# Kernel optimization log

Hardware: AMD Instinct MI355X
Metric: run time of the kernel (lower is better)

The kernel has to match this reference:

```python
import jax, jax.numpy as jnp
import numpy as np
import math

D = 256
N = 2048
B = 8
N_PLUS_1 = 2048  # masked index (1-based) in the score matrix


def setup_inputs() -> dict:
    key = jax.random.key(0)
    k1, k2, k3, k4, k5 = jax.random.split(key, 5)
    scale = 1.0 / math.sqrt(D)
    return {
        "Z_in": jax.random.normal(k1, (B, D + 1, N), dtype=jnp.float32),
        "A_l": jax.random.normal(k2, (D, D), dtype=jnp.float32) * scale,
        "r_l": jax.random.normal(k3, (1,), dtype=jnp.float32),
        "B_l": jax.random.normal(k4, (D, D), dtype=jnp.float32) * scale,
        "C_l": jax.random.normal(k5, (D, D), dtype=jnp.float32) * scale,
    }


def reference(Z_in, A_l, r_l, B_l, C_l):
    # Z_in: (B, d+1, N)
    X = Z_in[:, :D, :]   # (B, d, N)
    Y = Z_in[:, D:, :]   # (B, 1, N)
    U = jnp.einsum('ij,bjn->bin', B_l, X)  # (B, d, N)
    W = jnp.einsum('ij,bjn->bin', C_l, X)  # (B, d, N)
    scores = jnp.einsum('bdn,bdm->bnm', U, W)  # (B, N, N) = U^T W
    att = jax.nn.relu(scores)                  # h_type == 'relu'
    # zero the (n_plus_1-1, n_plus_1-1) diagonal entry of the attention core
    att = att.at[:, N_PLUS_1 - 1, N_PLUS_1 - 1].set(0.0)
    X_att = jnp.einsum('bdn,bnm->bdm', X, att)  # (B, d, N)
    X_out = X + jnp.einsum('ij,bjm->bim', A_l, X_att)
    Y_out = Y + r_l * jnp.einsum('bdn,bnm->bdm', Y, att)
    return jnp.concatenate([X_out, Y_out], axis=1)  # (B, d+1, N)
```

## Files before the change

### kernel.cpp

```cpp
#include <hip/hip_runtime.h>

#define D 256
#define N 2048
#define NB 8
#define ZSTRIDE (257 * 2048)

typedef __attribute__((ext_vector_type(8))) short short8;
typedef __attribute__((ext_vector_type(4))) short short4v;
typedef __attribute__((ext_vector_type(4))) float f32x4;

#define MFMA(a, b, c) __builtin_amdgcn_mfma_f32_16x16x32_bf16((a), (b), (c), 0, 0, 0)

#define GLOAD_LDS16(g, s) __builtin_amdgcn_global_load_lds( \
    (const __attribute__((address_space(1))) void*)(g),     \
    (__attribute__((address_space(3))) void*)(s), 16, 0, 0)

#define VMCNT(Nstr) asm volatile("s_waitcnt vmcnt(" Nstr ")" ::: "memory")
#define BAR() __builtin_amdgcn_s_barrier()

__device__ __forceinline__ short f2bf(float f) {
    unsigned u = __builtin_bit_cast(unsigned, f);
    u += 0x7fffu + ((u >> 16) & 1u);
    return (short)(u >> 16);
}
__device__ __forceinline__ float bf2f(short s) {
    unsigned u = ((unsigned)(unsigned short)s) << 16;
    return __builtin_bit_cast(float, u);
}

__global__ __launch_bounds__(256) void prep_small(
    const float* __restrict__ B_l, const float* __restrict__ C_l,
    const float* __restrict__ A_l, const float* __restrict__ Z,
    short* __restrict__ G, short* __restrict__ Ab, short* __restrict__ Yb,
    float* __restrict__ accY, int zeroAcc)
{
    int blk = blockIdx.x, tid = threadIdx.x;
    if (blk < 256) {
        float s = 0.f;
        #pragma unroll 8
        for (int k = 0; k < 256; ++k)
            s += B_l[k * 256 + blk] * C_l[k * 256 + tid];
        G[blk * 256 + tid] = f2bf(s);
    } else if (blk < 320) {
        int base = (blk - 256) * 1024 + tid;
        #pragma unroll
        for (int r = 0; r < 4; ++r) {
            int idx = base + r * 256;
            Ab[idx] = f2bf(A_l[idx]);
        }
    } else if (blk < 336) {
        int base = (blk - 320) * 1024 + tid;
        #pragma unroll
        for (int r = 0; r < 4; ++r) {
            int idx = base + r * 256;
            int b = idx >> 11, n = idx & 2047;
            Yb[idx] = f2bf(Z[(size_t)b * ZSTRIDE + 256 * N + n]);
        }
    } else if (zeroAcc) {
        int i = (blk - 336) * 256 + tid;
        f32x4 z = {0.f, 0.f, 0.f, 0.f};
        *(f32x4*)(accY + (size_t)i * 4) = z;
    }
}

__global__ __launch_bounds__(256) void transpose_kernel(
    const float* __restrict__ Z, short* __restrict__ Xt)
{
    typedef __attribute__((ext_vector_type(4))) float f4;
    __shared__ short t[64][68];
    int blk = blockIdx.x;
    int b = blk & 7;
    int dt = (blk >> 3) & 3;
    int nt = blk >> 5;
    int d0 = dt * 64, n0 = nt * 64;
    const float* ZB = Z + (size_t)b * ZSTRIDE;
    int tid = threadIdx.x;
    #pragma unroll
    for (int k = 0; k < 4; ++k) {
        int f = tid + k * 256;
        int r = f >> 4, c4 = f & 15;
        f4 v = *(const f4*)(ZB + (size_t)(d0 + r) * N + n0 + c4 * 4);
        #pragma unroll
        for (int j = 0; j < 4; ++j) t[r][c4 * 4 + j] = f2bf(v[j]);
    }
    __syncthreads();
    short* XtB = Xt + (size_t)b * (N * D);
    #pragma unroll
    for (int k = 0; k < 2; ++k) {
        int f = tid + k * 256;
        int n = f >> 3, c8 = f & 7;
        short8 v;
        #pragma unroll
        for (int j = 0; j < 8; ++j) v[j] = t[c8 * 8 + j][n];
        *(short8*)(XtB + (size_t)(n0 + n) * D + d0 + c8 * 8) = v;
    }
}

__global__ __launch_bounds__(512, 4) void prep_gemm2(
    const short* __restrict__ Xt, const short* __restrict__ G,
    const short* __restrict__ Ab, short* __restrict__ Wt, short* __restrict__ Px)
{
    __shared__ __align__(16) char smem[65536];
    typedef short TileT[128][64];
    TileT* As = (TileT*)smem;
    TileT* Bs = (TileT*)(smem + 32768);

    int blk = blockIdx.x;
    int half = blk >> 8;
    int r0 = blk & 255;
    int b = r0 >> 5;
    int idx = r0 & 31;

    const short* Arows;
    const short* Brows;
    short* Cout;
    size_t cstride;
    int row_base, col_base;
    if (half == 0) {
        row_base = (idx & 15) << 7;
        col_base = (idx >> 4) << 7;
        Arows = Xt + (size_t)b * (N * D);
        Brows = G;
        Cout  = Wt + (size_t)b * (N * D);
        cstride = D;
    } else {
        row_base = (idx & 1) << 7;
        col_base = (idx >> 1) << 7;
        Arows = Ab;
        Brows = Xt + (size_t)b * (N * D);
        Cout  = Px + (size_t)b * (D * N);
        cstride = N;
    }

    int tid = threadIdx.x;
    int w = tid >> 6, l = tid & 63;
    int l16 = l & 15, lq = l >> 4;
    int wm = w >> 2, wn = w & 3;
    int lrow8 = l >> 3, lc = l & 7;

    auto STAGE = [&](const short* base, int row0g, int kt, TileT* dst) {
        #pragma unroll
        for (int i = 0; i < 2; ++i) {
            int rloc = i * 64 + w * 8;
            int row = rloc + lrow8;
            const char* src = (const char*)(base + (size_t)(row0g + row) * D)
                              + kt * 128 + ((lc ^ (row & 7)) * 16);
            GLOAD_LDS16(src, &(*dst)[rloc][0]);
        }
    };

    f32x4 zero4 = {0.f, 0.f, 0.f, 0.f};
    f32x4 acc[4][2];
    #pragma unroll
    for (int mi = 0; mi < 4; ++mi)
        #pragma unroll
        for (int ni = 0; ni < 2; ++ni) acc[mi][ni] = zero4;

    STAGE(Arows, row_base, 0, &As[0]);
    STAGE(Brows, col_base, 0, &Bs[0]);

    int buf = 0;
    #pragma unroll
    for (int kt = 0; kt < 4; ++kt) {
        if (kt < 3) {
            STAGE(Arows, row_base, kt + 1, &As[buf ^ 1]);
            STAGE(Brows, col_base, kt + 1, &Bs[buf ^ 1]);
            VMCNT("4");
        } else {
            VMCNT("0");
        }
        BAR();
        __builtin_amdgcn_s_setprio(1);
        #pragma unroll
        for (int ks = 0; ks < 2; ++ks) {
            short8 af[4], bf[2];
            #pragma unroll
            for (int mi = 0; mi < 4; ++mi) {
                int r = wm * 64 + mi * 16 + l16;
                af[mi] = *(const short8*)(&As[buf][r][(ks * 32 + lq * 8) ^ ((r & 7) << 3)]);
            }
            #pragma unroll
            for (int ni = 0; ni < 2; ++ni) {
                int r = wn * 32 + ni * 16 + l16;
                bf[ni] = *(const short8*)(&Bs[buf][r][(ks * 32 + lq * 8) ^ ((r & 7) << 3)]);
            }
            #pragma unroll
            for (int mi = 0; mi < 4; ++mi)
                #pragma unroll
                for (int ni = 0; ni < 2; ++ni)
                    acc[mi][ni] = MFMA(af[mi], bf[ni], acc[mi][ni]);
        }
        __builtin_amdgcn_s_setprio(0);
        BAR();
        buf ^= 1;
    }

    short* cq = (short*)smem + (size_t)w * (64 * 40);
    #pragma unroll
    for (int mi = 0; mi < 4; ++mi)
        #pragma unroll
        for (int ni = 0; ni < 2; ++ni)
            #pragma unroll
            for (int rg = 0; rg < 4; ++rg)
                cq[(mi * 16 + lq * 4 + rg) * 40 + ni * 16 + l16] =
                    f2bf(acc[mi][ni][rg]);
    #pragma unroll
    for (int p = 0; p < 4; ++p) {
        int row = p * 16 + (l >> 2), c8 = l & 3;
        short8 v = *(const short8*)(&cq[row * 40 + c8 * 8]);
        *(short8*)(Cout + (size_t)(row_base + wm * 64 + row) * cstride +
                   col_base + wn * 32 + c8 * 8) = v;
    }
}

__global__ __launch_bounds__(512, 4) void scores_kernel(
    const short* __restrict__ Xt, const short* __restrict__ Wt,
    const short* __restrict__ Yb, short* __restrict__ attT,
    float* __restrict__ accY, int bBase, int nbMask, int nbShift)
{
    __shared__ __align__(16) char smem[77824];
    typedef short ATile[128][32];
    typedef short BTile[256][32];
    ATile* As = (ATile*)smem;
    BTile* Bs = (BTile*)(smem + 16384);
    short* scratch = (short*)(smem + 49152);

    int blk = blockIdx.x;
    int b_local = blk & nbMask;
    int idx = blk >> nbShift;
    int m_base = (idx & 15) << 7;
    int nsup = (idx >> 4) << 9;
    int b = bBase + b_local;

    int tid = threadIdx.x;
    int w = tid >> 6, l = tid & 63;
    int l16 = l & 15, lq = l >> 4;
    int wm = w >> 2, wn = w & 3;
    int lr4 = l >> 2, lc4 = l & 3;

    const short* WtB = Wt + (size_t)b * (N * D);
    const short* XtB = Xt + (size_t)b * (N * D);
    const short* YbB = Yb + (size_t)b * N;
    float* accYB = accY + (size_t)b * N;
    short* attTB = attT + (size_t)b_local * N * N;

    auto STAGE_A = [&](int kt, int bi) {
        int row = w * 16 + lr4;
        const char* src = (const char*)(WtB + (size_t)(m_base + row) * D)
                          + kt * 64 + ((lc4 ^ ((row >> 1) & 3)) * 16);
        GLOAD_LDS16(src, &As[bi][w * 16][0]);
    };
    auto STAGE_B = [&](int s, int kt, int bi) {
        #pragma unroll
        for (int i = 0; i < 2; ++i) {
            int row = i * 128 + w * 16 + lr4;
            const char* src = (const char*)(XtB + (size_t)(nsup + s * 256 + row) * D)
                              + kt * 64 + ((lc4 ^ ((row >> 1) & 3)) * 16);
            GLOAD_LDS16(src, &Bs[bi][i * 128 + w * 16][0]);
        }
    };

    f32x4 zero4 = {0.f, 0.f, 0.f, 0.f};
    f32x4 acc[4][4];
    #pragma unroll
    for (int mi = 0; mi < 4; ++mi)
        #pragma unroll
        for (int ni = 0; ni < 4; ++ni) acc[mi][ni] = zero4;

    STAGE_A(0, 0);
    STAGE_B(0, 0, 0);

    for (int t = 0; t < 16; ++t) {
        int kt = t & 7;
        int s = t >> 3;
        int buf = t & 1;
        if (t < 15) {
            int t1 = t + 1;
            STAGE_A(t1 & 7, t1 & 1);
            STAGE_B(t1 >> 3, t1 & 7, t1 & 1);
            VMCNT("3");
        } else {
            VMCNT("0");
        }
        BAR();
        __builtin_amdgcn_s_setprio(1);
        {
            short8 af[4], bf[4];
            #pragma unroll
            for (int mi = 0; mi < 4; ++mi) {
                int r = wm * 64 + mi * 16 + l16;
                af[mi] = *(const short8*)(&As[buf][r][(lq ^ ((r >> 1) & 3)) * 8]);
            }
            #pragma unroll
            for (int ni = 0; ni < 4; ++ni) {
                int r = wn * 64 + ni * 16 + l16;
                bf[ni] = *(const short8*)(&Bs[buf][r][(lq ^ ((r >> 1) & 3)) * 8]);
            }
            #pragma unroll
            for (int mi = 0; mi < 4; ++mi)
                #pragma unroll
                for (int ni = 0; ni < 4; ++ni)
                    acc[mi][ni] = MFMA(af[mi], bf[ni], acc[mi][ni]);
        }
        __builtin_amdgcn_s_setprio(0);
        BAR();

        if (kt == 7) {
            int n_base = nsup + s * 256;
            bool corner = (m_base == 1920) && (n_base == 1792);
            #pragma unroll
            for (int mi = 0; mi < 4; ++mi)
                #pragma unroll
                for (int ni = 0; ni < 4; ++ni)
                    #pragma unroll
                    for (int rg = 0; rg < 4; ++rg) {
                        float v = acc[mi][ni][rg];
                        v = v > 0.f ? v : 0.f;
                        if (corner) {
                            int gm = m_base + wm * 64 + mi * 16 + lq * 4 + rg;
                            int gn = n_base + wn * 64 + ni * 16 + l16;
                            if (gm == N - 1 && gn == N - 1) v = 0.f;
                        }
                        acc[mi][ni][rg] = v;
                    }
            {
                float yv[4];
                #pragma unroll
                for (int ni = 0; ni < 4; ++ni)
                    yv[ni] = bf2f(YbB[n_base + wn * 64 + ni * 16 + l16]);
                #pragma unroll
                for (int mi = 0; mi < 4; ++mi)
                    #pragma unroll
                    for (int rg = 0; rg < 4; ++rg) {
                        float sY = acc[mi][0][rg] * yv[0] + acc[mi][1][rg] * yv[1]
                                 + acc[mi][2][rg] * yv[2] + acc[mi][3][rg] * yv[3];
                        sY += __shfl_xor(sY, 1);
                        sY += __shfl_xor(sY, 2);
                        sY += __shfl_xor(sY, 4);
                        sY += __shfl_xor(sY, 8);
                        if (l16 == 0)
                            atomicAdd(&accYB[m_base + wm * 64 + mi * 16 + lq * 4 + rg], sY);
                    }
            }
            {
                short* sq = scratch + (size_t)w * (64 * 28);
                #pragma unroll
                for (int h = 0; h < 4; ++h) {
                    #pragma unroll
                    for (int mi = 0; mi < 4; ++mi)
                        #pragma unroll
                        for (int rg = 0; rg < 4; ++rg)
                            sq[(mi * 16 + lq * 4 + rg) * 28 + l16] =
                                f2bf(acc[mi][h][rg]);
                    #pragma unroll
                    for (int p = 0; p < 2; ++p) {
                        int row = p * 32 + (l >> 1), c8 = l & 1;
                        short8 v = *(const short8*)(&sq[row * 28 + c8 * 8]);
                        *(short8*)(attTB + (size_t)(m_base + wm * 64 + row) * N +
                                   n_base + wn * 64 + h * 16 + c8 * 8) = v;
                    }
                }
            }
            #pragma unroll
            for (int mi = 0; mi < 4; ++mi)
                #pragma unroll
                for (int ni = 0; ni < 4; ++ni) acc[mi][ni] = zero4;
        }
    }
}

__global__ __launch_bounds__(512, 4) void pv_kernel(
    const float* __restrict__ Z, const short* __restrict__ Px,
    const short* __restrict__ attT, const float* __restrict__ accY,
    const float* __restrict__ r_l, float* __restrict__ out,
    int bBase, int nbMask, int nbShift)
{
    __shared__ __align__(16) char smem[49152];
    typedef short ATile[64][64];
    typedef short BTile[128][64];
    ATile* As = (ATile*)smem;
    BTile* Bs = (BTile*)(smem + 16384);

    int blk = blockIdx.x;
    int b_local = blk & nbMask;
    int idx = blk >> nbShift;
    int d_base = (idx & 3) << 6;
    int m_base = (idx >> 2) << 7;
    int b = bBase + b_local;

    int tid = threadIdx.x;
    int w = tid >> 6, l = tid & 63;
    int l16 = l & 15, lq = l >> 4;
    int wd = w >> 2, wm = w & 3;
    int lrow8 = l >> 3, lc = l & 7;

    const short* PxB = Px + (size_t)b * (D * N);
    const short* attTB = attT + (size_t)b_local * N * N;

    auto STAGE_A = [&](int kt, ATile* dst) {
        int rloc = w * 8;
        int row = rloc + lrow8;
        const char* src = (const char*)(PxB + (size_t)(d_base + row) * N)
                          + kt * 128 + ((lc ^ (row & 7)) * 16);
        GLOAD_LDS16(src, &(*dst)[rloc][0]);
    };
    auto STAGE_B = [&](int kt, BTile* dst) {
        #pragma unroll
        for (int i = 0; i < 2; ++i) {
            int rloc = i * 64 + w * 8;
            int row = rloc + lrow8;
            const char* src = (const char*)(attTB + (size_t)(m_base + row) * N)
                              + kt * 128 + ((lc ^ (row & 7)) * 16);
            GLOAD_LDS16(src, &(*dst)[rloc][0]);
        }
    };

    f32x4 zero4 = {0.f, 0.f, 0.f, 0.f};
    f32x4 acc[2][2];
    #pragma unroll
    for (int di = 0; di < 2; ++di)
        #pragma unroll
        for (int mj = 0; mj < 2; ++mj) acc[di][mj] = zero4;

    STAGE_A(0, &As[0]);
    STAGE_B(0, &Bs[0]);

    int buf = 0;
    for (int kt = 0; kt < 32; ++kt) {
        if (kt < 31) {
            STAGE_A(kt + 1, &As[buf ^ 1]);
            STAGE_B(kt + 1, &Bs[buf ^ 1]);
            VMCNT("3");
        } else {
            VMCNT("0");
        }
        BAR();
        __builtin_amdgcn_s_setprio(1);
        #pragma unroll
        for (int ks = 0; ks < 2; ++ks) {
            short8 af[2], bf[2];
            #pragma unroll
            for (int di = 0; di < 2; ++di) {
                int r = wd * 32 + di * 16 + l16;
                af[di] = *(const short8*)(&As[buf][r][(ks * 32 + lq * 8) ^ ((r & 7) << 3)]);
            }
            #pragma unroll
            for (int mj = 0; mj < 2; ++mj) {
                int r = wm * 32 + mj * 16 + l16;
                bf[mj] = *(const short8*)(&Bs[buf][r][(ks * 32 + lq * 8) ^ ((r & 7) << 3)]);
            }
            #pragma unroll
            for (int di = 0; di < 2; ++di)
                #pragma unroll
                for (int mj = 0; mj < 2; ++mj)
                    acc[di][mj] = MFMA(af[di], bf[mj], acc[di][mj]);
        }
        __builtin_amdgcn_s_setprio(0);
        BAR();
        buf ^= 1;
    }

    #pragma unroll
    for (int di = 0; di < 2; ++di)
        #pragma unroll
        for (int mj = 0; mj < 2; ++mj)
            #pragma unroll
            for (int rg = 0; rg < 4; ++rg) {
                int dd = d_base + wd * 32 + di * 16 + lq * 4 + rg;
                int mm = m_base + wm * 32 + mj * 16 + l16;
                size_t off = (size_t)b * ZSTRIDE + (size_t)dd * N + mm;
                out[off] = Z[off] + acc[di][mj][rg];
            }

    if (d_base == 0 && tid < 128) {
        int mm = m_base + tid;
        size_t off = (size_t)b * ZSTRIDE + (size_t)256 * N + mm;
        out[off] = Z[off] + r_l[0] * accY[(size_t)b * N + mm];
    }
}

__global__ __launch_bounds__(512, 4) void fused_kernel(
    const float* __restrict__ Z, const short* __restrict__ Xt,
    const short* __restrict__ Wt, const short* __restrict__ Px,
    const short* __restrict__ Yb, const float* __restrict__ r_l,
    float* __restrict__ out)
{
    __shared__ __align__(16) short xtsA[32][256];
    __shared__ __align__(16) short xtsB[32][256];
    __shared__ __align__(16) short attA[64][36];
    __shared__ __align__(16) short attB[64][36];

    int blk = blockIdx.x;
    int b = blk & 7;
    int m_base = (blk >> 3) << 6;
    int tid = threadIdx.x;
    int w = tid >> 6, l = tid & 63;
    int l16 = l & 15, lq = l >> 4;

    const short* XtB = Xt + (size_t)b * (N * D);
    const short* WtB = Wt + (size_t)b * (N * D);
    const short* PxB = Px + (size_t)b * (D * N);
    const short* YbB = Yb + b * N;

    int mi = w >> 1;
    int nj = w & 1;

    short8 a_wt[8];
    {
        const short* ap = WtB + (size_t)(m_base + 16 * mi + l16) * D + lq * 8;
        #pragma unroll
        for (int ks = 0; ks < 8; ++ks)
            a_wt[ks] = *(const short8*)(ap + ks * 32);
    }

    f32x4 zero4 = {0.f, 0.f, 0.f, 0.f};
    f32x4 accX[2][4];
    #pragma unroll
    for (int di = 0; di < 2; ++di)
        #pragma unroll
        for (int mj = 0; mj < 4; ++mj) accX[di][mj] = zero4;

    float accY = 0.f;
    int ym = tid >> 3, yseg = tid & 7;

    auto STAGE = [&](int it, short (*dst)[256]) {
        #pragma unroll
        for (int r = 0; r < 2; ++r) {
            int row  = r * 16 + 2 * w + (l >> 5);
            int colb = ((l & 31) * 16) ^ ((row & 7) << 4);
            const char* src = (const char*)(XtB + (size_t)(it * 32 + row) * D) + colb;
            GLOAD_LDS16(src, &dst[r * 16 + 2 * w][0]);
        }
    };

    auto BODY = [&](int it, short (*xrd)[256], short (*xst)[256], short (*atw)[36]) {
        int n_base = it * 32;
        if (it + 1 < 64) STAGE(it + 1, xst);
        short8 px[2];
        #pragma unroll
        for (int di = 0; di < 2; ++di)
            px[di] = *(const short8*)(PxB + (size_t)(32 * w + 16 * di + l16) * N +
                                      n_base + lq * 8);
        short4v yv = *(const short4v*)(YbB + n_base + yseg * 4);
        f32x4 sa = zero4;
        #pragma unroll
        for (int ks = 0; ks < 8; ++ks) {
            int colsh = (ks * 32 + lq * 8) ^ ((l16 & 7) << 3);
            short8 xb = *(const short8*)(&xrd[16 * nj + l16][colsh]);
            sa = MFMA(a_wt[ks], xb, sa);
        }
        {
            int nn = 16 * nj + l16;
            #pragma unroll
            for (int rg = 0; rg < 4; ++rg) {
                int mm = 16 * mi + lq * 4 + rg;
                float v = sa[rg] > 0.f ? sa[rg] : 0.f;
                if ((m_base + mm == N - 1) && (n_base + nn == N - 1)) v = 0.f;
                atw[mm][nn] = f2bf(v);
            }
        }
        __syncthreads();
        #pragma unroll
        for (int mj = 0; mj < 4; ++mj) {
            short8 bfr = *(const short8*)(&atw[16 * mj + l16][lq * 8]);
            #pragma unroll
            for (int di = 0; di < 2; ++di)
                accX[di][mj] = MFMA(px[di], bfr, accX[di][mj]);
        }
        {
            short4v av = *(const short4v*)(&atw[ym][yseg * 4]);
            #pragma unroll
            for (int j = 0; j < 4; ++j)
                accY += bf2f(av[j]) * bf2f(yv[j]);
        }
    };

    STAGE(0, xtsA);
    __syncthreads();
    for (int it2 = 0; it2 < 32; ++it2) {
        BODY(2 * it2,     xtsA, xtsB, attA);
        BODY(2 * it2 + 1, xtsB, xtsA, attB);
    }

    #pragma unroll
    for (int di = 0; di < 2; ++di)
        #pragma unroll
        for (int mj = 0; mj < 4; ++mj)
            #pragma unroll
            for (int rg = 0; rg < 4; ++rg) {
                int dd = 32 * w + 16 * di + lq * 4 + rg;
                int mm = m_base + 16 * mj + l16;
                size_t off = (size_t)b * ZSTRIDE + (size_t)dd * N + mm;
                out[off] = Z[off] + accX[di][mj][rg];
            }
    accY += __shfl_xor(accY, 1);
    accY += __shfl_xor(accY, 2);
    accY += __shfl_xor(accY, 4);
    if (yseg == 0) {
        float r = r_l[0];
        int mm = m_base + ym;
        size_t off = (size_t)b * ZSTRIDE + (size_t)256 * N + mm;
        out[off] = Z[off] + r * accY;
    }
}

extern "C" void kernel_launch(void* const* d_in, const int* in_sizes, int n_in,
                              void* d_out, int out_size, void* d_ws, size_t ws_size,
                              hipStream_t stream) {
    const float* Z   = (const float*)d_in[0];
    const float* A_l = (const float*)d_in[1];
    const float* r_l = (const float*)d_in[2];
    const float* B_l = (const float*)d_in[3];
    const float* C_l = (const float*)d_in[4];
    float* out = (float*)d_out;

    char* ws = (char*)d_ws;
    short* G    = (short*)(ws);
    short* Ab   = (short*)(ws + 131072);
    short* Xt   = (short*)(ws + 262144);
    short* Wt   = (short*)(ws + 8650752);
    short* Px   = (short*)(ws + 17039360);
    short* Yb   = (short*)(ws + 25427968);
    float* accY = (float*)(ws + 25460736);
    short* attT = (short*)(ws + 25526272);

    const size_t baseNeed = 25526272;
    const size_t attSz = (size_t)N * N * 2;
    int NBCH = 8, nbShift = 3;
    while (NBCH > 1 && baseNeed + (size_t)NBCH * attSz > ws_size) { NBCH >>= 1; --nbShift; }
    bool decomposed = (baseNeed + (size_t)NBCH * attSz <= ws_size);

    prep_small<<<352, 256, 0, stream>>>(B_l, C_l, A_l, Z, G, Ab, Yb,
                                        accY, decomposed ? 1 : 0);
    transpose_kernel<<<1024, 256, 0, stream>>>(Z, Xt);
    prep_gemm2<<<512, 512, 0, stream>>>(Xt, G, Ab, Wt, Px);

    if (decomposed) {
        int nbMask = NBCH - 1;
        for (int c = 0; c < NB / NBCH; ++c) {
            int bBase = c * NBCH;
            scores_kernel<<<NBCH * 64, 512, 0, stream>>>(
                Xt, Wt, Yb, attT, accY, bBase, nbMask, nbShift);
            pv_kernel<<<NBCH * 64, 512, 0, stream>>>(
                Z, Px, attT, accY, r_l, out, bBase, nbMask, nbShift);
        }
    } else {
        fused_kernel<<<256, 512, 0, stream>>>(Z, Xt, Wt, Px, Yb, r_l, out);
    }
}
```

Measured before the change: 93.91 us.

## Pre-tile and pre-swizzle Xt and Wt so scores kernel loads contiguous blocks

The transpose kernel now also writes a second copy of X^T in a tile-major, pre-swizzled layout (128-row by 32-column blocks with XOR slot swizzle). When decomposed, prep_gemm2 writes Wt in the same tiled layout. The scores kernel can then stage each LDS tile with fully contiguous 1KB-per-wave global loads instead of strided row gathers with per-lane address math. The cost is an extra 8MB write of Xt2 and a larger workspace requirement, which could lower the number of batches processed per chunk.

```diff
diff --git a/kernel.cpp b/kernel.cpp
--- a/kernel.cpp
+++ b/kernel.cpp
@@ -64,15 +64,15 @@
 }
 
 __global__ __launch_bounds__(256) void transpose_kernel(
-    const float* __restrict__ Z, short* __restrict__ Xt)
+    const float* __restrict__ Z, short* __restrict__ Xt, short* __restrict__ Xt2)
 {
     typedef __attribute__((ext_vector_type(4))) float f4;
     __shared__ short t[64][68];
     int blk = blockIdx.x;
     int b = blk & 7;
     int dt = (blk >> 3) & 3;
-    int nt = blk >> 5;
-    int d0 = dt * 64, n0 = nt * 64;
+    int nt4 = blk >> 5;
+    int d0 = dt * 64, n0 = nt4 * 64;
     const float* ZB = Z + (size_t)b * ZSTRIDE;
     int tid = threadIdx.x;
     #pragma unroll
@@ -85,6 +85,7 @@
     }
     __syncthreads();
     short* XtB = Xt + (size_t)b * (N * D);
+    short* Xt2B = Xt2 + (size_t)b * (N * D);
     #pragma unroll
     for (int k = 0; k < 2; ++k) {
         int f = tid + k * 256;
@@ -92,13 +93,20 @@
         short8 v;
         #pragma unroll
         for (int j = 0; j < 8; ++j) v[j] = t[c8 * 8 + j][n];
-        *(short8*)(XtB + (size_t)(n0 + n) * D + d0 + c8 * 8) = v;
+        int gn = n0 + n;
+        int d = d0 + c8 * 8;
+        *(short8*)(XtB + (size_t)gn * D + d) = v;
+        int nt = gn >> 7, mrow = gn & 127;
+        int kt = d >> 5, q = (d & 31) >> 3;
+        int slot = q ^ ((mrow >> 1) & 3);
+        *(short8*)(Xt2B + (size_t)nt * 32768 + kt * 4096 + mrow * 32 + slot * 8) = v;
     }
 }
 
 __global__ __launch_bounds__(512, 4) void prep_gemm2(
     const short* __restrict__ Xt, const short* __restrict__ G,
-    const short* __restrict__ Ab, short* __restrict__ Wt, short* __restrict__ Px)
+    const short* __restrict__ Ab, short* __restrict__ Wt, short* __restrict__ Px,
+    int tiledWt)
 {
     __shared__ __align__(16) char smem[65536];
     typedef short TileT[128][64];
@@ -113,23 +121,17 @@
 
     const short* Arows;
     const short* Brows;
-    short* Cout;
-    size_t cstride;
     int row_base, col_base;
     if (half == 0) {
         row_base = (idx & 15) << 7;
         col_base = (idx >> 4) << 7;
         Arows = Xt + (size_t)b * (N * D);
         Brows = G;
-        Cout  = Wt + (size_t)b * (N * D);
-        cstride = D;
     } else {
         row_base = (idx & 1) << 7;
         col_base = (idx >> 1) << 7;
         Arows = Ab;
         Brows = Xt + (size_t)b * (N * D);
-        Cout  = Px + (size_t)b * (D * N);
-        cstride = N;
     }
 
     int tid = threadIdx.x;
@@ -204,17 +206,34 @@
             for (int rg = 0; rg < 4; ++rg)
                 cq[(mi * 16 + lq * 4 + rg) * 40 + ni * 16 + l16] =
                     f2bf(acc[mi][ni][rg]);
-    #pragma unroll
-    for (int p = 0; p < 4; ++p) {
-        int row = p * 16 + (l >> 2), c8 = l & 3;
-        short8 v = *(const short8*)(&cq[row * 40 + c8 * 8]);
-        *(short8*)(Cout + (size_t)(row_base + wm * 64 + row) * cstride +
-                   col_base + wn * 32 + c8 * 8) = v;
+    if (half == 0 && tiledWt) {
+        short* base2 = Wt + (size_t)b * (N * D) + (size_t)(row_base >> 7) * 32768;
+        #pragma unroll
+        for (int p = 0; p < 4; ++p) {
+            int row = p * 16 + (l >> 2), c8 = l & 3;
+            short8 v = *(const short8*)(&cq[row * 40 + c8 * 8]);
+            int mrow = wm * 64 + row;
+            int kt2 = (col_base >> 5) + wn;
+            int slot = c8 ^ ((mrow >> 1) & 3);
+            *(short8*)(base2 + (size_t)kt2 * 4096 + mrow * 32 + slot * 8) = v;
+        }
+    } else {
+        short* Cout;
+        size_t cstride;
+        if (half == 0) { Cout = Wt + (size_t)b * (N * D); cstride = D; }
+        else           { Cout = Px + (size_t)b * (D * N); cstride = N; }
+        #pragma unroll
+        for (int p = 0; p < 4; ++p) {
+            int row = p * 16 + (l >> 2), c8 = l & 3;
+            short8 v = *(const short8*)(&cq[row * 40 + c8 * 8]);
+            *(short8*)(Cout + (size_t)(row_base + wm * 64 + row) * cstride +
+                       col_base + wn * 32 + c8 * 8) = v;
+        }
     }
 }
 
 __global__ __launch_bounds__(512, 4) void scores_kernel(
-    const short* __restrict__ Xt, const short* __restrict__ Wt,
+    const short* __restrict__ Xt2, const short* __restrict__ Wt2,
     const short* __restrict__ Yb, short* __restrict__ attT,
     float* __restrict__ accY, int bBase, int nbMask, int nbShift)
 {
@@ -236,26 +255,23 @@
     int w = tid >> 6, l = tid & 63;
     int l16 = l & 15, lq = l >> 4;
     int wm = w >> 2, wn = w & 3;
-    int lr4 = l >> 2, lc4 = l & 3;
-
-    const short* WtB = Wt + (size_t)b * (N * D);
-    const short* XtB = Xt + (size_t)b * (N * D);
+
+    const short* Wt2B = Wt2 + (size_t)b * (N * D) + (size_t)(m_base >> 7) * 32768;
+    const short* Xt2B = Xt2 + (size_t)b * (N * D);
     const short* YbB = Yb + (size_t)b * N;
     float* accYB = accY + (size_t)b * N;
     short* attTB = attT + (size_t)b_local * N * N;
+    int nt0base = nsup >> 7;
 
     auto STAGE_A = [&](int kt, int bi) {
-        int row = w * 16 + lr4;
-        const char* src = (const char*)(WtB + (size_t)(m_base + row) * D)
-                          + kt * 64 + ((lc4 ^ ((row >> 1) & 3)) * 16);
+        const char* src = (const char*)Wt2B + kt * 8192 + w * 1024 + l * 16;
         GLOAD_LDS16(src, &As[bi][w * 16][0]);
     };
     auto STAGE_B = [&](int s, int kt, int bi) {
         #pragma unroll
         for (int i = 0; i < 2; ++i) {
-            int row = i * 128 + w * 16 + lr4;
-            const char* src = (const char*)(XtB + (size_t)(nsup + s * 256 + row) * D)
-                              + kt * 64 + ((lc4 ^ ((row >> 1) & 3)) * 16);
+            const char* src = (const char*)Xt2B +
+                (size_t)(nt0base + s * 2 + i) * 65536 + kt * 8192 + w * 1024 + l * 16;
             GLOAD_LDS16(src, &Bs[bi][i * 128 + w * 16][0]);
         }
     };
@@ -622,9 +638,10 @@
     short* Px   = (short*)(ws + 17039360);
     short* Yb   = (short*)(ws + 25427968);
     float* accY = (float*)(ws + 25460736);
-    short* attT = (short*)(ws + 25526272);
-
-    const size_t baseNeed = 25526272;
+    short* Xt2  = (short*)(ws + 25526272);
+    short* attT = (short*)(ws + 33914880);
+
+    const size_t baseNeed = 33914880;
     const size_t attSz = (size_t)N * N * 2;
     int NBCH = 8, nbShift = 3;
     while (NBCH > 1 && baseNeed + (size_t)NBCH * attSz > ws_size) { NBCH >>= 1; --nbShift; }
@@ -632,15 +649,15 @@
 
     prep_small<<<352, 256, 0, stream>>>(B_l, C_l, A_l, Z, G, Ab, Yb,
                                         accY, decomposed ? 1 : 0);
-    transpose_kernel<<<1024, 256, 0, stream>>>(Z, Xt);
-    prep_gemm2<<<512, 512, 0, stream>>>(Xt, G, Ab, Wt, Px);
+    transpose_kernel<<<1024, 256, 0, stream>>>(Z, Xt, Xt2);
+    prep_gemm2<<<512, 512, 0, stream>>>(Xt, G, Ab, Wt, Px, decomposed ? 1 : 0);
 
     if (decomposed) {
         int nbMask = NBCH - 1;
         for (int c = 0; c < NB / NBCH; ++c) {
             int bBase = c * NBCH;
             scores_kernel<<<NBCH * 64, 512, 0, stream>>>(
-                Xt, Wt, Yb, attT, accY, bBase, nbMask, nbShift);
+                Xt2, Wt, Yb, attT, accY, bBase, nbMask, nbShift);
             pv_kernel<<<NBCH * 64, 512, 0, stream>>>(
                 Z, Px, attT, accY, r_l, out, bBase, nbMask, nbShift);
         }
```

New measurement: 94.14 us. Within noise of the previous version (+0.3%).
